# Performance work log

Measured on AMD Instinct MI355X. Metric: run time of the kernel, lower is better.

The kernel has to match this reference:

```python
import jax, jax.numpy as jnp
import numpy as np

B, N, D_NODE, D_EDGE, D_GRAPH = 2, 1024, 128, 16, 128
MID, OUT = 64, 128


def _linear_params(key, fan_in, fan_out):
    # haiku Linear default: truncated-normal(stddev=1/sqrt(fan_in)) weight, zero bias
    w = jax.random.normal(key, (fan_in, fan_out), dtype=jnp.float32) / np.sqrt(fan_in)
    b = jnp.zeros((fan_out,), dtype=jnp.float32)
    return w, b


def setup_inputs() -> dict:
    key = jax.random.key(0)
    ks = jax.random.split(key, 12)
    features = jax.random.normal(ks[0], (B, N, D_NODE), dtype=jnp.float32)
    e_features = jax.random.normal(ks[1], (B, N, N, D_EDGE), dtype=jnp.float32)
    g_features = jax.random.normal(ks[2], (B, D_GRAPH), dtype=jnp.float32)
    adj = jax.random.randint(ks[3], (B, N, N), 0, 2).astype(jnp.float32)
    # ensure self-loops so every row has at least one valid neighbor
    adj = jnp.maximum(adj, jnp.eye(N, dtype=jnp.float32)[None])
    Wm, bm = _linear_params(ks[4], D_NODE, OUT)
    Wskip, bskip = _linear_params(ks[5], D_NODE, OUT)
    W1, b1 = _linear_params(ks[6], D_NODE, MID)
    W2, b2 = _linear_params(ks[7], D_NODE, MID)
    We, be = _linear_params(ks[8], D_EDGE, MID)
    Wg, bg = _linear_params(ks[9], D_GRAPH, MID)
    Wa, ba = _linear_params(ks[10], MID, 1)
    return dict(features=features, e_features=e_features, g_features=g_features,
                adj=adj, Wm=Wm, bm=bm, Wskip=Wskip, bskip=bskip,
                W1=W1, b1=b1, W2=W2, b2=b2, We=We, be=be, Wg=Wg, bg=bg,
                Wa=Wa, ba=ba)


def reference(features, e_features, g_features, adj,
              Wm, bm, Wskip, bskip, W1, b1, W2, b2, We, be, Wg, bg, Wa, ba):
    # bias mask: 0 where edge exists, -1e9 where not
    bias_mat = (adj - 1.0) * 1e9  # (b,n,n)

    values = features @ Wm + bm          # (b,n,out)
    pre_att_1 = features @ W1 + b1       # (b,n,mid) -> per-target j
    pre_att_2 = features @ W2 + b2       # (b,n,mid) -> per-source i
    pre_att_e = e_features @ We + be     # (b,n,n,mid)
    pre_att_g = g_features @ Wg + bg     # (b,mid)

    # pre_att[b,i,j] = p1[b,j] + p2[b,i] + pe[b,i,j] + pg[b]
    pre_att = (pre_att_1[:, None, :, :] + pre_att_2[:, :, None, :]
               + pre_att_e + pre_att_g[:, None, None, :])  # (b,n,n,mid)

    logits = jnp.squeeze(jax.nn.leaky_relu(pre_att) @ Wa + ba, axis=-1)  # (b,n,n)
    coefs = jax.nn.softmax(logits + bias_mat, axis=-1)                   # (b,n,n)

    ret = jnp.matmul(coefs, values)       # (b,n,out)
    ret = ret + (features @ Wskip + bskip)  # residual
    return jax.nn.relu(ret)               # activation=relu
```

## Files before the change

### kernel.cpp

```cpp
#include <hip/hip_runtime.h>
#include <hip/hip_bf16.h>
#include <cstdint>

#define B_   2
#define N_   1024
#define DN_  128
#define DE_  16
#define DG_  128
#define MID_ 64
#define OUT_ 128
#define TI_  4
#define PR_ROWS 4

typedef short bf16x8 __attribute__((ext_vector_type(8)));
typedef float f32x4  __attribute__((ext_vector_type(4)));

__device__ inline short f2bf(float f) {
    union { float f; unsigned u; } v; v.f = f;
    unsigned r = v.u + 0x7FFFu + ((v.u >> 16) & 1u);
    return (short)(unsigned short)(r >> 16);
}

__device__ inline unsigned pk2(float lo, float hi) {
    union { __hip_bfloat162 h; unsigned u; } p;
    p.h = __float22bfloat162_rn(make_float2(lo, hi));
    return p.u;
}

__global__ void __launch_bounds__(384) prep_all(
    const float* __restrict__ features, const float* __restrict__ g_features,
    const float* __restrict__ Wm, const float* __restrict__ bm,
    const float* __restrict__ Wskip, const float* __restrict__ bskip,
    const float* __restrict__ W1, const float* __restrict__ b1,
    const float* __restrict__ W2, const float* __restrict__ b2,
    const float* __restrict__ We, const float* __restrict__ be,
    const float* __restrict__ Wg, const float* __restrict__ bg,
    float* __restrict__ values, float* __restrict__ skipo,
    float* __restrict__ P1x, float* __restrict__ p2,
    float* __restrict__ pg, short* __restrict__ We_frag)
{
    const int t   = threadIdx.x;
    const int blk = blockIdx.x;

    if (blk == 512) {
        for (int e = t; e < 4 * 64 * 8; e += 384) {
            const int c    = e >> 9;
            const int lane = (e >> 3) & 63;
            const int j    = e & 7;
            const int quad = lane >> 4, s = lane & 15;
            short v = 0;
            if (quad < 2) v = f2bf(We[(quad * 8 + j) * MID_ + c * 16 + s]);
            We_frag[e] = v;
        }
        return;
    }
    if (blk == 513) {
        if (t < MID_) {
            float a0 = bg[t], a1 = bg[t];
            for (int k = 0; k < DG_; ++k) {
                const float w = Wg[k * MID_ + t];
                a0 += g_features[k] * w;
                a1 += g_features[DG_ + k] * w;
            }
            pg[t] = a0; pg[MID_ + t] = a1;
        }
        return;
    }

    const int r0 = blk * PR_ROWS;
    __shared__ float feat[PR_ROWS][DN_];
    for (int idx = t; idx < PR_ROWS * DN_; idx += 384)
        feat[idx >> 7][idx & 127] = features[(size_t)r0 * DN_ + idx];
    __syncthreads();

    const float* W; int c, stride; float base; float* outp; int ostride;
    if (t < 128) {
        W = Wm;    c = t;       stride = OUT_; base = bm[c];
        outp = values + (size_t)r0 * OUT_ + c; ostride = OUT_;
    } else if (t < 256) {
        W = Wskip; c = t - 128; stride = OUT_; base = bskip[c];
        outp = skipo + (size_t)r0 * OUT_ + c;  ostride = OUT_;
    } else if (t < 320) {
        W = W1;    c = t - 256; stride = MID_; base = b1[c] + be[c];
        outp = P1x + (size_t)r0 * MID_ + c;    ostride = MID_;
    } else {
        W = W2;    c = t - 320; stride = MID_; base = b2[c];
        outp = p2 + (size_t)r0 * MID_ + c;     ostride = MID_;
    }

    float acc[PR_ROWS] = {};
    for (int k = 0; k < DN_; ++k) {
        const float w = W[k * stride + c];
        #pragma unroll
        for (int q = 0; q < PR_ROWS; ++q) acc[q] += feat[q][k] * w;
    }
    #pragma unroll
    for (int q = 0; q < PR_ROWS; ++q) outp[q * ostride] = acc[q] + base;
}

__global__ void __launch_bounds__(256) gat_main(
    const float* __restrict__ e_features, const float* __restrict__ adj,
    const short* __restrict__ We_frag, const float* __restrict__ Wa,
    const float* __restrict__ values, const float* __restrict__ skipo,
    const float* __restrict__ P1x, const float* __restrict__ p2,
    const float* __restrict__ pg, float* __restrict__ out)
{
    const int t    = threadIdx.x;
    const int wv   = t >> 6;
    const int l    = t & 63;
    const int quad = l >> 4;
    const int s    = l & 15;
    const int r    = blockIdx.x;
    const int b    = (r >> 2) & 1;
    const int i0   = (((r >> 3) << 2) | (r & 3)) * TI_;

    __shared__ float lgP[TI_][N_];
    __shared__ float redv[TI_][16][36];
    __shared__ float sinv[TI_];

    bf16x8 bfr[4];
    float  wa_r[4], p2i[TI_][4];
    #pragma unroll
    for (int c = 0; c < 4; ++c) {
        bfr[c]  = *(const bf16x8*)&We_frag[(c * 64 + l) * 8];
        wa_r[c] = Wa[c * 16 + s];
        const float pgc = pg[b * MID_ + c * 16 + s];
        #pragma unroll
        for (int ii = 0; ii < TI_; ++ii)
            p2i[ii][c] = p2[((size_t)(b * N_ + i0 + ii)) * MID_ + c * 16 + s] + pgc;
    }
    const size_t erow0 = (size_t)(b * N_ + i0) * N_;

    float4 eA[TI_][2];
    if (quad < 2) {
        #pragma unroll
        for (int ii = 0; ii < TI_; ++ii) {
            const float* ep = &e_features[(erow0 + (size_t)ii * N_ + wv * 16 + s) * DE_ + quad * 8];
            eA[ii][0] = *(const float4*)ep;
            eA[ii][1] = *(const float4*)(ep + 4);
        }
    }
    for (int it = 0; it < 16; ++it) {
        const int tile = wv + it * 4;
        const int j0   = tile * 16;

        unsigned af[TI_][4];
        #pragma unroll
        for (int ii = 0; ii < TI_; ++ii) {
            if (quad < 2) {
                af[ii][0] = pk2(eA[ii][0].x, eA[ii][0].y);
                af[ii][1] = pk2(eA[ii][0].z, eA[ii][0].w);
                af[ii][2] = pk2(eA[ii][1].x, eA[ii][1].y);
                af[ii][3] = pk2(eA[ii][1].z, eA[ii][1].w);
            } else {
                af[ii][0] = af[ii][1] = af[ii][2] = af[ii][3] = 0u;
            }
        }
        if (it < 15) {
            const int jn = (tile + 4) * 16;
            if (quad < 2) {
                #pragma unroll
                for (int ii = 0; ii < TI_; ++ii) {
                    const float* ep = &e_features[(erow0 + (size_t)ii * N_ + jn + s) * DE_ + quad * 8];
                    eA[ii][0] = *(const float4*)ep;
                    eA[ii][1] = *(const float4*)(ep + 4);
                }
            }
        }
        float base[4][4];
        {
            const float* pb = &P1x[((size_t)(b * N_) + j0 + quad * 4) * MID_ + s];
            #pragma unroll
            for (int c = 0; c < 4; ++c)
                #pragma unroll
                for (int rr = 0; rr < 4; ++rr)
                    base[c][rr] = pb[rr * MID_ + c * 16];
        }
        #pragma unroll
        for (int ii = 0; ii < TI_; ++ii) {
            union { unsigned u[4]; bf16x8 v; } a;
            a.u[0] = af[ii][0]; a.u[1] = af[ii][1];
            a.u[2] = af[ii][2]; a.u[3] = af[ii][3];
            f32x4 acc[4];
            #pragma unroll
            for (int c = 0; c < 4; ++c) {
                acc[c] = (f32x4){0.f, 0.f, 0.f, 0.f};
                acc[c] = __builtin_amdgcn_mfma_f32_16x16x32_bf16(a.v, bfr[c], acc[c], 0, 0, 0);
            }
            float tt[4];
            #pragma unroll
            for (int rr = 0; rr < 4; ++rr) {
                float x0 = acc[0][rr] + base[0][rr] + p2i[ii][0];
                float x1 = acc[1][rr] + base[1][rr] + p2i[ii][1];
                float x2 = acc[2][rr] + base[2][rr] + p2i[ii][2];
                float x3 = acc[3][rr] + base[3][rr] + p2i[ii][3];
                x0 = fmaxf(x0, 0.01f * x0);
                x1 = fmaxf(x1, 0.01f * x1);
                x2 = fmaxf(x2, 0.01f * x2);
                x3 = fmaxf(x3, 0.01f * x3);
                tt[rr] = x0 * wa_r[0] + x1 * wa_r[1] + x2 * wa_r[2] + x3 * wa_r[3];
            }
            #pragma unroll
            for (int o = 1; o < 16; o <<= 1) {
                tt[0] += __shfl_xor(tt[0], o);
                tt[1] += __shfl_xor(tt[1], o);
                tt[2] += __shfl_xor(tt[2], o);
                tt[3] += __shfl_xor(tt[3], o);
            }
            if (s < 4) lgP[ii][j0 + quad * 4 + s] = tt[s];
        }
    }
    __syncthreads();

    {
        const size_t arb = (size_t)(b * N_ + i0 + wv) * N_;
        float4 lv[4], av[4];
        #pragma unroll
        for (int q = 0; q < 4; ++q) {
            lv[q] = *(const float4*)&lgP[wv][l * 4 + 256 * q];
            av[q] = *(const float4*)&adj[arb + l * 4 + 256 * q];
        }
        const float NEG = -3.4e38f;
        float m = NEG;
        #pragma unroll
        for (int q = 0; q < 4; ++q) {
            m = fmaxf(m, av[q].x > 0.f ? lv[q].x : NEG);
            m = fmaxf(m, av[q].y > 0.f ? lv[q].y : NEG);
            m = fmaxf(m, av[q].z > 0.f ? lv[q].z : NEG);
            m = fmaxf(m, av[q].w > 0.f ? lv[q].w : NEG);
        }
        #pragma unroll
        for (int o = 1; o < 64; o <<= 1) m = fmaxf(m, __shfl_xor(m, o));
        float sum = 0.f;
        #pragma unroll
        for (int q = 0; q < 4; ++q) {
            float4 e4;
            e4.x = av[q].x > 0.f ? __expf(lv[q].x - m) : 0.f;
            e4.y = av[q].y > 0.f ? __expf(lv[q].y - m) : 0.f;
            e4.z = av[q].z > 0.f ? __expf(lv[q].z - m) : 0.f;
            e4.w = av[q].w > 0.f ? __expf(lv[q].w - m) : 0.f;
            *(float4*)&lgP[wv][l * 4 + 256 * q] = e4;
            sum += (e4.x + e4.y) + (e4.z + e4.w);
        }
        #pragma unroll
        for (int o = 1; o < 64; o <<= 1) sum += __shfl_xor(sum, o);
        if (l == 0) sinv[wv] = 1.0f / sum;
    }
    __syncthreads();

    const int cg = l & 15, jp = l >> 4, ch0 = cg * 8;
    float acc[TI_][8] = {};
    const float* vb = values + (size_t)b * N_ * OUT_ + ch0;
    for (int k = 0; k < 64; ++k) {
        const int j = wv * 4 + jp + k * 16;
        float cw[TI_];
        #pragma unroll
        for (int ii = 0; ii < TI_; ++ii) cw[ii] = lgP[ii][j];
        const float* vp = vb + (size_t)j * OUT_;
        const float4 v0 = *(const float4*)vp;
        const float4 v1 = *(const float4*)(vp + 4);
        const float vv[8] = {v0.x, v0.y, v0.z, v0.w, v1.x, v1.y, v1.z, v1.w};
        #pragma unroll
        for (int ii = 0; ii < TI_; ++ii)
            #pragma unroll
            for (int kk = 0; kk < 8; ++kk)
                acc[ii][kk] += cw[ii] * vv[kk];
    }
    #pragma unroll
    for (int ii = 0; ii < TI_; ++ii)
        #pragma unroll
        for (int kk = 0; kk < 8; ++kk) {
            acc[ii][kk] += __shfl_xor(acc[ii][kk], 16);
            acc[ii][kk] += __shfl_xor(acc[ii][kk], 32);
        }
    if (l < 16) {
        #pragma unroll
        for (int ii = 0; ii < TI_; ++ii)
            #pragma unroll
            for (int q = 0; q < 2; ++q) {
                float4 w4 = make_float4(acc[ii][q * 4], acc[ii][q * 4 + 1],
                                        acc[ii][q * 4 + 2], acc[ii][q * 4 + 3]);
                *(float4*)&redv[wv][l][ii * 8 + q * 4] = w4;
            }
    }
    __syncthreads();
    {
        const int ch = t & 127, g = ch >> 3, kk = ch & 7;
        const int iib = t >> 7;
        #pragma unroll
        for (int p = 0; p < 2; ++p) {
            const int ii = iib + p * 2;
            const float sum = redv[0][g][ii * 8 + kk] + redv[1][g][ii * 8 + kk]
                            + redv[2][g][ii * 8 + kk] + redv[3][g][ii * 8 + kk];
            const size_t ob = ((size_t)(b * N_ + i0 + ii)) * OUT_ + ch;
            out[ob] = fmaxf(sum * sinv[ii] + skipo[ob], 0.f);
        }
    }
}

extern "C" void kernel_launch(void* const* d_in, const int* in_sizes, int n_in,
                              void* d_out, int out_size, void* d_ws, size_t ws_size,
                              hipStream_t stream) {
    const float* features   = (const float*)d_in[0];
    const float* e_features = (const float*)d_in[1];
    const float* g_features = (const float*)d_in[2];
    const float* adj        = (const float*)d_in[3];
    const float* Wm    = (const float*)d_in[4];
    const float* bm    = (const float*)d_in[5];
    const float* Wskip = (const float*)d_in[6];
    const float* bskip = (const float*)d_in[7];
    const float* W1    = (const float*)d_in[8];
    const float* b1    = (const float*)d_in[9];
    const float* W2    = (const float*)d_in[10];
    const float* b2    = (const float*)d_in[11];
    const float* We    = (const float*)d_in[12];
    const float* be    = (const float*)d_in[13];
    const float* Wg    = (const float*)d_in[14];
    const float* bg    = (const float*)d_in[15];
    const float* Wa    = (const float*)d_in[16];
    float* out = (float*)d_out;

    float* ws      = (float*)d_ws;
    float* values  = ws;
    float* skipo   = ws + 262144;
    float* P1x     = ws + 524288;
    float* p2      = ws + 655360;
    float* pg      = ws + 786432;
    short* We_frag = (short*)(ws + 786560);

    prep_all<<<B_ * N_ / PR_ROWS + 2, 384, 0, stream>>>(
        features, g_features, Wm, bm, Wskip, bskip, W1, b1, W2, b2,
        We, be, Wg, bg, values, skipo, P1x, p2, pg, We_frag);
    gat_main<<<B_ * N_ / TI_, 256, 0, stream>>>(
        e_features, adj, We_frag, Wa, values, skipo, P1x, p2, pg, out);
}
```

Baseline: 298.4 us.

## Use 512-thread blocks in gat_main, splitting tiles and softmax across eight waves

```diff
diff --git a/kernel.cpp b/kernel.cpp
--- a/kernel.cpp
+++ b/kernel.cpp
@@ -98,7 +98,7 @@
     for (int q = 0; q < PR_ROWS; ++q) outp[q * ostride] = acc[q] + base;
 }
 
-__global__ void __launch_bounds__(256) gat_main(
+__global__ void __launch_bounds__(512, 4) gat_main(
     const float* __restrict__ e_features, const float* __restrict__ adj,
     const short* __restrict__ We_frag, const float* __restrict__ Wa,
     const float* __restrict__ values, const float* __restrict__ skipo,
@@ -115,8 +115,10 @@
     const int i0   = (((r >> 3) << 2) | (r & 3)) * TI_;
 
     __shared__ float lgP[TI_][N_];
-    __shared__ float redv[TI_][16][36];
+    __shared__ float redv[8][16][36];
     __shared__ float sinv[TI_];
+    __shared__ float pmax[8];
+    __shared__ float psum[8];
 
     bf16x8 bfr[4];
     float  wa_r[4], p2i[TI_][4];
@@ -140,8 +142,8 @@
             eA[ii][1] = *(const float4*)(ep + 4);
         }
     }
-    for (int it = 0; it < 16; ++it) {
-        const int tile = wv + it * 4;
+    for (int it = 0; it < 8; ++it) {
+        const int tile = wv + it * 8;
         const int j0   = tile * 16;
 
         unsigned af[TI_][4];
@@ -156,8 +158,8 @@
                 af[ii][0] = af[ii][1] = af[ii][2] = af[ii][3] = 0u;
             }
         }
-        if (it < 15) {
-            const int jn = (tile + 4) * 16;
+        if (it < 7) {
+            const int jn = (tile + 8) * 16;
             if (quad < 2) {
                 #pragma unroll
                 for (int ii = 0; ii < TI_; ++ii) {
@@ -213,17 +215,19 @@
     __syncthreads();
 
     {
-        const size_t arb = (size_t)(b * N_ + i0 + wv) * N_;
-        float4 lv[4], av[4];
-        #pragma unroll
-        for (int q = 0; q < 4; ++q) {
-            lv[q] = *(const float4*)&lgP[wv][l * 4 + 256 * q];
-            av[q] = *(const float4*)&adj[arb + l * 4 + 256 * q];
+        const int rw = wv & 3, h = wv >> 2;
+        const int c0 = h * 512 + l * 4;
+        const size_t arb = (size_t)(b * N_ + i0 + rw) * N_;
+        float4 lv[2], av[2];
+        #pragma unroll
+        for (int q = 0; q < 2; ++q) {
+            lv[q] = *(const float4*)&lgP[rw][c0 + 256 * q];
+            av[q] = *(const float4*)&adj[arb + c0 + 256 * q];
         }
         const float NEG = -3.4e38f;
         float m = NEG;
         #pragma unroll
-        for (int q = 0; q < 4; ++q) {
+        for (int q = 0; q < 2; ++q) {
             m = fmaxf(m, av[q].x > 0.f ? lv[q].x : NEG);
             m = fmaxf(m, av[q].y > 0.f ? lv[q].y : NEG);
             m = fmaxf(m, av[q].z > 0.f ? lv[q].z : NEG);
@@ -231,28 +235,32 @@
         }
         #pragma unroll
         for (int o = 1; o < 64; o <<= 1) m = fmaxf(m, __shfl_xor(m, o));
+        if (l == 0) pmax[wv] = m;
+        __syncthreads();
+        m = fmaxf(pmax[rw], pmax[4 + rw]);
         float sum = 0.f;
         #pragma unroll
-        for (int q = 0; q < 4; ++q) {
+        for (int q = 0; q < 2; ++q) {
             float4 e4;
             e4.x = av[q].x > 0.f ? __expf(lv[q].x - m) : 0.f;
             e4.y = av[q].y > 0.f ? __expf(lv[q].y - m) : 0.f;
             e4.z = av[q].z > 0.f ? __expf(lv[q].z - m) : 0.f;
             e4.w = av[q].w > 0.f ? __expf(lv[q].w - m) : 0.f;
-            *(float4*)&lgP[wv][l * 4 + 256 * q] = e4;
+            *(float4*)&lgP[rw][c0 + 256 * q] = e4;
             sum += (e4.x + e4.y) + (e4.z + e4.w);
         }
         #pragma unroll
         for (int o = 1; o < 64; o <<= 1) sum += __shfl_xor(sum, o);
-        if (l == 0) sinv[wv] = 1.0f / sum;
-    }
-    __syncthreads();
+        if (l == 0) psum[wv] = sum;
+        __syncthreads();
+        if (t < TI_) sinv[t] = 1.0f / (psum[t] + psum[t + 4]);
+    }
 
     const int cg = l & 15, jp = l >> 4, ch0 = cg * 8;
     float acc[TI_][8] = {};
     const float* vb = values + (size_t)b * N_ * OUT_ + ch0;
-    for (int k = 0; k < 64; ++k) {
-        const int j = wv * 4 + jp + k * 16;
+    for (int k = 0; k < 32; ++k) {
+        const int j = wv * 4 + jp + k * 32;
         float cw[TI_];
         #pragma unroll
         for (int ii = 0; ii < TI_; ++ii) cw[ii] = lgP[ii][j];
@@ -286,15 +294,12 @@
     __syncthreads();
     {
         const int ch = t & 127, g = ch >> 3, kk = ch & 7;
-        const int iib = t >> 7;
-        #pragma unroll
-        for (int p = 0; p < 2; ++p) {
-            const int ii = iib + p * 2;
-            const float sum = redv[0][g][ii * 8 + kk] + redv[1][g][ii * 8 + kk]
-                            + redv[2][g][ii * 8 + kk] + redv[3][g][ii * 8 + kk];
-            const size_t ob = ((size_t)(b * N_ + i0 + ii)) * OUT_ + ch;
-            out[ob] = fmaxf(sum * sinv[ii] + skipo[ob], 0.f);
-        }
+        const int ii = t >> 7;
+        float sum = redv[0][g][ii * 8 + kk];
+        #pragma unroll
+        for (int w = 1; w < 8; ++w) sum += redv[w][g][ii * 8 + kk];
+        const size_t ob = ((size_t)(b * N_ + i0 + ii)) * OUT_ + ch;
+        out[ob] = fmaxf(sum * sinv[ii] + skipo[ob], 0.f);
     }
 }
 
@@ -331,6 +336,6 @@
     prep_all<<<B_ * N_ / PR_ROWS + 2, 384, 0, stream>>>(
         features, g_features, Wm, bm, Wskip, bskip, W1, b1, W2, b2,
         We, be, Wg, bg, values, skipo, P1x, p2, pg, We_frag);
-    gat_main<<<B_ * N_ / TI_, 256, 0, stream>>>(
+    gat_main<<<B_ * N_ / TI_, 512, 0, stream>>>(
         e_features, adj, We_frag, Wa, values, skipo, P1x, p2, pg, out);
 }
```

Result: slower. 340.6 us (+14.2%).
